# Kernel tuning notes

Hardware: AMD Instinct MI355X
Metric: run time of the kernel (lower is better)

The kernel has to match this reference:

```python
import jax, jax.numpy as jnp
import numpy as np

NC = 80
REG = 16          # DFL bins per coordinate
CONF_THRES = 0.25
IOU_THRES = 0.45
MAX_DET = 300
TOPK = 1000       # fixed-size pre-NMS candidate pool (stand-in for max_nms=30000 with A=8400)
MAX_WH = 7680.0   # class offset for class-aware NMS
LEVELS = [(80, 80, 8.0), (40, 40, 16.0), (20, 20, 32.0)]  # (h, w, stride) for imgsz=640


def _make_anchors():
    """make_anchors: grid-cell centers (+0.5 offset) and per-anchor strides."""
    pts, strs = [], []
    for h, w, s in LEVELS:
        sx = jnp.arange(w, dtype=jnp.float32) + 0.5
        sy = jnp.arange(h, dtype=jnp.float32) + 0.5
        gy, gx = jnp.meshgrid(sy, sx, indexing='ij')
        pts.append(jnp.stack([gx, gy], -1).reshape(-1, 2))
        strs.append(jnp.full((h * w,), s, dtype=jnp.float32))
    return jnp.concatenate(pts).T, jnp.concatenate(strs)  # [2, A], [A]


def _box_iou(b):  # b: [K, 4] xyxy -> [K, K] pairwise IoU
    area = (b[:, 2] - b[:, 0]) * (b[:, 3] - b[:, 1])
    lt = jnp.maximum(b[:, None, :2], b[None, :, :2])
    rb = jnp.minimum(b[:, None, 2:], b[None, :, 2:])
    wh = jnp.clip(rb - lt, 0.0)
    inter = wh[..., 0] * wh[..., 1]
    return inter / (area[:, None] + area[None, :] - inter + 1e-7)


def _nms_keep(iou, valid):
    """Greedy NMS over score-sorted candidates: keep[i] iff valid and no earlier kept box overlaps > thr."""
    K = iou.shape[0]
    idx = jnp.arange(K)
    def body(keep, i):
        sup = jnp.any((iou[i] > IOU_THRES) & keep & (idx < i))
        return keep.at[i].set(valid[i] & jnp.logical_not(sup)), None
    keep, _ = jax.lax.scan(body, jnp.zeros(K, dtype=bool), idx)
    return keep


def _forward(preds, dfl_w):
    B, C, A = preds.shape
    # DFL decode: softmax over 16 bins, expectation with arange(16) weights (the 1x1 conv)
    box_logits = preds[:, :4 * REG].reshape(B, 4, REG, A)
    dist = jnp.einsum('bqra,r->bqa', jax.nn.softmax(box_logits, axis=2), dfl_w)  # [B,4,A] ltrb
    anc, strd = _make_anchors()
    lt, rb = dist[:, :2], dist[:, 2:]
    x1y1 = anc[None] - lt
    x2y2 = anc[None] + rb
    c_xy = (x1y1 + x2y2) / 2
    wh = x2y2 - x1y1
    dbox = jnp.concatenate([c_xy, wh], axis=1) * strd  # dist2bbox(xywh) * stride, [B,4,A]
    cls = jax.nn.sigmoid(preds[:, 4 * REG:])           # [B,NC,A]
    # xywh2xyxy
    cx, cy, w, h = dbox[:, 0], dbox[:, 1], dbox[:, 2], dbox[:, 3]
    boxes = jnp.stack([cx - w / 2, cy - h / 2, cx + w / 2, cy + h / 2], axis=-1)  # [B,A,4]
    conf = jnp.max(cls, axis=1)      # [B,A]
    j = jnp.argmax(cls, axis=1)      # [B,A]
    score = jnp.where(conf > CONF_THRES, conf, -1.0)
    top_s, top_i = jax.lax.top_k(score, TOPK)                               # [B,K]
    tb = jnp.take_along_axis(boxes, top_i[..., None], axis=1)               # [B,K,4]
    tj = jnp.take_along_axis(j, top_i, axis=1)                              # [B,K]
    valid = top_s > CONF_THRES
    ob = tb + (tj.astype(preds.dtype) * MAX_WH)[..., None]                  # class-offset boxes
    iou = jax.vmap(_box_iou)(ob)                                            # [B,K,K]
    keep = jax.vmap(_nms_keep)(iou, valid)                                  # [B,K]
    sel = jnp.where(keep, top_s, -1e9)
    order = jnp.argsort(-sel, axis=1)[:, :MAX_DET]                          # kept, score-sorted
    fb = jnp.take_along_axis(tb, order[..., None], axis=1)
    fs = jnp.take_along_axis(top_s, order, axis=1)
    fj = jnp.take_along_axis(tj, order, axis=1).astype(preds.dtype)
    fv = jnp.take_along_axis(keep, order, axis=1)
    out = jnp.concatenate([fb, fs[..., None], fj[..., None]], axis=-1)
    return out * fv[..., None].astype(preds.dtype)                          # [B,300,6]


def setup_inputs() -> dict:
    key = jax.random.key(0)
    k1, _ = jax.random.split(key)
    preds = jax.random.normal(k1, (32, 4 * REG + NC, 8400), dtype=jnp.float32)
    dfl_w = jnp.arange(REG, dtype=jnp.float32)
    return {"preds": preds, "dfl_w": dfl_w}


def reference(preds, dfl_w):
    return _forward(preds, dfl_w)
```

## Files before the change

### kernel.cpp

```cpp
#include <hip/hip_runtime.h>
#include <cstdint>
#include <cstddef>

typedef unsigned long long u64;
typedef unsigned int u32;

#define A_TOT   8400
#define NCLS    80
#define KSLOT   1024
#define NCHUNK  9
#define TOPK_N  1000
#define MAXDET  300
#define OUT_STRIDE (MAXDET * 6)


__device__ __forceinline__ float sig32(float x) {
#pragma clang fp contract(off)
    float e = (float)exp(-(double)x);
    float t = 1.0f + e;
    return 1.0f / t;
}

__device__ __forceinline__ u32 key_hi_from_score(float s) {
    u32 u = __float_as_uint(s);
    return (u & 0x80000000u) ? ~u : (u | 0x80000000u);
}
__device__ __forceinline__ float score_from_key_hi(u32 t) {
    u32 u = (t & 0x80000000u) ? (t ^ 0x80000000u) : ~t;
    return __uint_as_float(u);
}

__global__ __launch_bounds__(256) void k_decode(const float* __restrict__ preds,
                                                u64* __restrict__ key_raw,
                                                float4* __restrict__ dbox) {
#pragma clang fp contract(off)
    __shared__ float tile[2][16][256];
    int b = blockIdx.y;
    int a0 = blockIdx.x * 256;
    int t = threadIdx.x;
    int a = a0 + t;
    int nA = A_TOT - a0; if (nA > 256) nA = 256;
    int p4max = nA >> 2;
    const float* pb = preds + (size_t)b * 144 * A_TOT;

    int sr[4], sp[4];
#pragma unroll
    for (int k = 0; k < 4; ++k) { int f = t + 256 * k; sr[k] = f >> 6; sp[k] = f & 63; }

    float4 regs[4];
    auto gload = [&](int ch0) {
#pragma unroll
        for (int k = 0; k < 4; ++k) {
            if (sp[k] < p4max)
                regs[k] = *(const float4*)(pb + (size_t)(ch0 + sr[k]) * A_TOT + a0 + 4 * sp[k]);
            else
                regs[k] = make_float4(0.f, 0.f, 0.f, 0.f);
        }
    };
    auto dswrite = [&](int buf) {
#pragma unroll
        for (int k = 0; k < 4; ++k)
            *(float4*)&tile[buf][sr[k]][4 * sp[k]] = regs[k];
    };

    float d[4] = {0.f, 0.f, 0.f, 0.f};
    float m = -3.0e38f, m2 = -3.0e38f;
    int jm = 0;

    gload(0); dswrite(0); __syncthreads();
    gload(16);

    for (int cb = 0; cb < 9; ++cb) {
        int buf = cb & 1;
        if (t < nA) {
            float x[16];
#pragma unroll
            for (int r = 0; r < 16; ++r) x[r] = tile[buf][r][t];
            if (cb < 4) {
                float mx = x[0];
#pragma unroll
                for (int r = 1; r < 16; ++r) mx = fmaxf(mx, x[r]);
                float e[16], s = 0.f;
#pragma unroll
                for (int r = 0; r < 16; ++r) { e[r] = expf(x[r] - mx); s = s + e[r]; }
                float dd = 0.f;
#pragma unroll
                for (int r = 0; r < 16; ++r) { float pr = e[r] / s; dd = dd + pr * (float)r; }
                d[cb] = dd;
            } else {
                int cbase = (cb - 4) * 16;
#pragma unroll
                for (int r = 0; r < 16; ++r) {
                    int c = cbase + r;
                    float v = x[r];
                    if (v > m) { m2 = m; m = v; jm = c; }
                    else if (v > m2) { m2 = v; }
                }
            }
        }
        if (cb + 1 < 9) {
            __syncthreads();
            dswrite((cb + 1) & 1);
            if (cb + 2 < 9) gload((cb + 2) * 16);
            __syncthreads();
        }
    }

    if (t >= nA) return;

    const float* pc = pb + (size_t)64 * A_TOT + a;
    float conf; int cls = jm;
    if ((m - m2) < 1e-4f || m > 7.0f) {
        float sb = -1.0f; int jb = 0;
        for (int c = 0; c < NCLS; ++c) {
            float s = sig32(pc[(size_t)c * A_TOT]);
            if (s > sb) { sb = s; jb = c; }
        }
        conf = sb; cls = jb;
    } else {
        conf = sig32(m);
    }
    float score = (conf > 0.25f) ? conf : -1.0f;
    u32 hi = key_hi_from_score(score);
    u32 lo = ((0x3FFFu - (u32)a) << 7) | (u32)cls;
    key_raw[(size_t)b * A_TOT + a] = ((u64)hi << 32) | lo;

    int row, col; float stride;
    if (a < 6400)      { row = a / 80;          col = a % 80;          stride = 8.0f; }
    else if (a < 8000) { int aa = a - 6400; row = aa / 40; col = aa % 40; stride = 16.0f; }
    else               { int aa = a - 8000; row = aa / 20; col = aa % 20; stride = 32.0f; }
    float ax = (float)col + 0.5f;
    float ay = (float)row + 0.5f;
    float x1 = ax - d[0], y1 = ay - d[1];
    float x2 = ax + d[2], y2 = ay + d[3];
    float cx = (x1 + x2) / 2.0f, cy = (y1 + y2) / 2.0f;
    float w  = x2 - x1,          h  = y2 - y1;
    float4 db;
    db.x = cx * stride; db.y = cy * stride; db.z = w * stride; db.w = h * stride;
    dbox[(size_t)b * A_TOT + a] = db;
}

__global__ __launch_bounds__(1024) void k_chunksort(const u64* __restrict__ key_raw,
                                                    u64* __restrict__ key_sorted) {
    __shared__ u64 s[KSLOT];
    int b = blockIdx.y, ch = blockIdx.x, t = threadIdx.x;
    int a = ch * KSLOT + t;
    s[t] = (a < A_TOT) ? key_raw[(size_t)b * A_TOT + a] : 0ull;
    __syncthreads();
    for (int k = 2; k <= KSLOT; k <<= 1) {
        for (int j = k >> 1; j > 0; j >>= 1) {
            int ixj = t ^ j;
            if (ixj > t) {
                u64 x = s[t], y = s[ixj];
                bool descBlock = ((t & k) == 0);
                bool sw = descBlock ? (x < y) : (x > y);
                if (sw) { s[t] = y; s[ixj] = x; }
            }
            __syncthreads();
        }
    }
    key_sorted[((size_t)b * NCHUNK + ch) * KSLOT + t] = s[t];
}

__global__ __launch_bounds__(1024) void k_merge(const u64* __restrict__ key_sorted,
                                                u64* __restrict__ topk) {
    __shared__ u64 R[KSLOT];
    __shared__ u64 C[KSLOT];
    int b = blockIdx.x, t = threadIdx.x;
    R[t] = key_sorted[((size_t)b * NCHUNK) * KSLOT + t];
    for (int ch = 1; ch < NCHUNK; ++ch) {
        C[t] = key_sorted[((size_t)b * NCHUNK + ch) * KSLOT + t];
        __syncthreads();
        u64 r = R[t];
        u64 c = C[(KSLOT - 1) - t];
        u64 nv = (r > c) ? r : c;
        __syncthreads();
        R[t] = nv;
        __syncthreads();
        for (int j = KSLOT >> 1; j >= 1; j >>= 1) {
            int ixj = t ^ j;
            if (ixj > t) {
                u64 x = R[t], y = R[ixj];
                if (x < y) { R[t] = y; R[ixj] = x; }
            }
            __syncthreads();
        }
    }
    topk[(size_t)b * KSLOT + t] = R[t];
}

__global__ void k_prep(const float4* __restrict__ dbox, const u64* __restrict__ topk,
                       float* __restrict__ tb, float* __restrict__ ob,
                       float* __restrict__ area, u32* __restrict__ validf) {
#pragma clang fp contract(off)
    int slot = blockIdx.x * blockDim.x + threadIdx.x;
    int b = blockIdx.y;
    if (slot >= KSLOT) return;
    size_t si = (size_t)b * KSLOT + slot;
    u64 key = topk[si];
    u32 hi = (u32)(key >> 32);
    u32 lo = (u32)key;
    bool valid = (slot < TOPK_N) && (hi & 0x80000000u);
    if (!valid) {
        tb[si*4+0]=0.f; tb[si*4+1]=0.f; tb[si*4+2]=0.f; tb[si*4+3]=0.f;
        ob[si*4+0]=0.f; ob[si*4+1]=0.f; ob[si*4+2]=0.f; ob[si*4+3]=0.f;
        area[si] = 0.f; validf[si] = 0u;
        return;
    }
    int a   = 0x3FFF - (int)((lo >> 7) & 0x3FFFu);
    int cls = (int)(lo & 0x7Fu);

    float4 db = dbox[(size_t)b * A_TOT + a];
    float bx1 = db.x - db.z / 2.0f, by1 = db.y - db.w / 2.0f;
    float bx2 = db.x + db.z / 2.0f, by2 = db.y + db.w / 2.0f;
    tb[si*4+0] = bx1; tb[si*4+1] = by1; tb[si*4+2] = bx2; tb[si*4+3] = by2;

    float off = (float)cls * 7680.0f;
    float o0 = bx1 + off, o1 = by1 + off, o2 = bx2 + off, o3 = by2 + off;
    ob[si*4+0] = o0; ob[si*4+1] = o1; ob[si*4+2] = o2; ob[si*4+3] = o3;
    area[si] = (o2 - o0) * (o3 - o1);
    validf[si] = 1u;
}

__global__ __launch_bounds__(256) void k_matrix(const float* __restrict__ ob,
                                                const float* __restrict__ area,
                                                u64* __restrict__ masks) {
#pragma clang fp contract(off)
    __shared__ float4 sob[KSLOT];
    __shared__ float  sar[KSLOT];
    int b = blockIdx.y, rblk = blockIdx.x, tid = threadIdx.x;
    const float4* gob = (const float4*)(ob + (size_t)b * KSLOT * 4);
    const float*  gar = area + (size_t)b * KSLOT;
    for (int i = tid; i < KSLOT; i += blockDim.x) { sob[i] = gob[i]; sar[i] = gar[i]; }
    __syncthreads();

    int lane = tid & 63;
    int wave = tid >> 6;
    int i = rblk * 64 + lane;
    float4 bi = sob[i];
    float Ai = sar[i];

#pragma unroll
    for (int wl = 0; wl < 4; ++wl) {
        int w = wave * 4 + wl;
        u64 mword = 0ull;
        if (w >= rblk) {
            for (int bit = 0; bit < 64; ++bit) {
                int j = (w << 6) + bit;
                float4 bj = sob[j];
                float Aj = sar[j];
                float lt0 = fmaxf(bi.x, bj.x);
                float lt1 = fmaxf(bi.y, bj.y);
                float rb0 = fminf(bi.z, bj.z);
                float rb1 = fminf(bi.w, bj.w);
                float ww = fmaxf(rb0 - lt0, 0.0f);
                float hh = fmaxf(rb1 - lt1, 0.0f);
                float inter = ww * hh;
                float den = ((Ai + Aj) - inter) + 1e-7f;
                float iou = inter / den;
                if ((j > i) && (iou > 0.45f)) mword |= (1ull << bit);
            }
        }
        masks[((size_t)b * KSLOT + i) * 16 + w] = mword;
    }
}

__global__ __launch_bounds__(64) void k_scan(const u64* __restrict__ masks,
                                             const u32* __restrict__ validf,
                                             u64* __restrict__ keep) {
    __shared__ u64 rows[KSLOT];
    int b = blockIdx.x, lane = threadIdx.x;
    const char* base = (const char*)(masks + (size_t)b * KSLOT * 16);

    float4 r0, r1, r2, r3, r4, r5, r6, r7;
    {
        const float4* src = (const float4*)base;
        r0 = src[0*64 + lane]; r1 = src[1*64 + lane];
        r2 = src[2*64 + lane]; r3 = src[3*64 + lane];
        r4 = src[4*64 + lane]; r5 = src[5*64 + lane];
        r6 = src[6*64 + lane]; r7 = src[7*64 + lane];
    }

    u64 kw = 0ull;
    u64 rem = 0ull;
    int kept = 0;

    for (int w = 0; w < 16; ++w) {
        {
            float4* dst = (float4*)rows;
            dst[0*64 + lane] = r0; dst[1*64 + lane] = r1;
            dst[2*64 + lane] = r2; dst[3*64 + lane] = r3;
            dst[4*64 + lane] = r4; dst[5*64 + lane] = r5;
            dst[6*64 + lane] = r6; dst[7*64 + lane] = r7;
        }
        u32 vf = validf[(size_t)b * KSLOT + w * 64 + lane];
        u64 valid_w = __ballot(vf != 0u);
        __syncthreads();
        if (w < 15) {
            const float4* src = (const float4*)(base + (size_t)(w + 1) * 8192);
            r0 = src[0*64 + lane]; r1 = src[1*64 + lane];
            r2 = src[2*64 + lane]; r3 = src[3*64 + lane];
            r4 = src[4*64 + lane]; r5 = src[5*64 + lane];
            r6 = src[6*64 + lane]; r7 = src[7*64 + lane];
        }

        u64 live = valid_w & ~__shfl(rem, w);
        while (live) {
            int i = __ffsll(live) - 1;
            if (lane == w) kw |= (1ull << i);
            u64 m = (lane < 16) ? rows[i * 16 + lane] : 0ull;
            rem |= m;
            ++kept;
            if (kept >= MAXDET) break;
            live &= ~(__shfl(m, w) | (1ull << i));
        }
        if (kept >= MAXDET) break;
        __syncthreads();
    }
    if (lane < 16) keep[(size_t)b * 16 + lane] = kw;
}

__global__ __launch_bounds__(1024) void k_final(const u64* __restrict__ keep,
                                                const u64* __restrict__ topk,
                                                const float* __restrict__ tb,
                                                float* __restrict__ out) {
    __shared__ u64 kw[16];
    __shared__ int pref[16];
    int b = blockIdx.x, t = threadIdx.x;
    float* ob_ = out + (size_t)b * OUT_STRIDE;
    for (int i = t; i < OUT_STRIDE; i += blockDim.x) ob_[i] = 0.0f;
    if (t < 16) kw[t] = keep[(size_t)b * 16 + t];
    __syncthreads();
    if (t == 0) {
        int s = 0;
        for (int w = 0; w < 16; ++w) { pref[w] = s; s += __popcll(kw[w]); }
    }
    __syncthreads();
    int w = t >> 6, bit = t & 63;
    bool kp = (kw[w] >> bit) & 1ull;
    if (kp) {
        u64 below = (bit == 0) ? 0ull : (kw[w] & ((1ull << bit) - 1ull));
        int rank = pref[w] + __popcll(below);
        if (rank < MAXDET) {
            size_t si = (size_t)b * KSLOT + t;
            u64 key = topk[si];
            u32 hi = (u32)(key >> 32);
            u32 lo = (u32)key;
            float score = score_from_key_hi(hi);
            float clsf = (float)(lo & 0x7Fu);
            float* o = ob_ + rank * 6;
            o[0] = tb[si*4+0]; o[1] = tb[si*4+1];
            o[2] = tb[si*4+2]; o[3] = tb[si*4+3];
            o[4] = score; o[5] = clsf;
        }
    }
}

extern "C" void kernel_launch(void* const* d_in, const int* in_sizes, int n_in,
                              void* d_out, int out_size, void* d_ws, size_t ws_size,
                              hipStream_t stream) {
    const float* preds = (const float*)d_in[0];
    float* out = (float*)d_out;
    int B = in_sizes[0] / (144 * A_TOT);

    char* ws = (char*)d_ws;
    size_t off = 0;
    u64* key_raw    = (u64*)(ws + off); off += (size_t)B * A_TOT * 8;
    u64* key_sorted = (u64*)(ws + off); off += (size_t)B * NCHUNK * KSLOT * 8;
    u64* topk       = (u64*)(ws + off); off += (size_t)B * KSLOT * 8;
    float4* dbox    = (float4*)(ws + off); off += (size_t)B * A_TOT * 16;
    float* tb       = (float*)(ws + off); off += (size_t)B * KSLOT * 4 * 4;
    float* obuf     = (float*)(ws + off); off += (size_t)B * KSLOT * 4 * 4;
    float* area     = (float*)(ws + off); off += (size_t)B * KSLOT * 4;
    u32* validf     = (u32*)(ws + off); off += (size_t)B * KSLOT * 4;
    u64* masks      = (u64*)(ws + off); off += (size_t)B * KSLOT * 16 * 8;
    u64* keep       = (u64*)(ws + off); off += (size_t)B * 16 * 8;

    k_decode<<<dim3((A_TOT + 255) / 256, B), 256, 0, stream>>>(preds, key_raw, dbox);
    k_chunksort<<<dim3(NCHUNK, B), KSLOT, 0, stream>>>(key_raw, key_sorted);
    k_merge<<<B, KSLOT, 0, stream>>>(key_sorted, topk);
    k_prep<<<dim3(KSLOT / 256, B), 256, 0, stream>>>(dbox, topk, tb, obuf, area, validf);
    k_matrix<<<dim3(16, B), 256, 0, stream>>>(obuf, area, masks);
    k_scan<<<B, 64, 0, stream>>>(masks, validf, keep);
    k_final<<<B, 1024, 0, stream>>>(keep, topk, tb, out);
}
```

Measured before the change: 167.9 us.

## Replace bitonic chunk merge with merge-path tree selection fused with prep

The sequential 8-step bitonic merge of sorted chunks is replaced by a tree of merge-path rank selections. Each thread binary-searches for its output element when merging two sorted lists and keeps the top 1024. The prep kernel is fused into the same kernel, which removes one launch and the topk re-read. The first level reads global memory directly inside the binary search, which adds dependent latency, but far fewer barriers are needed.

```diff
diff --git a/kernel.cpp b/kernel.cpp
--- a/kernel.cpp
+++ b/kernel.cpp
@@ -28,6 +28,18 @@
 __device__ __forceinline__ float score_from_key_hi(u32 t) {
     u32 u = (t & 0x80000000u) ? (t ^ 0x80000000u) : ~t;
     return __uint_as_float(u);
+}
+
+__device__ __forceinline__ u64 mp_rank(const u64* __restrict__ A,
+                                       const u64* __restrict__ B, int t) {
+    int lo = 0, hi = t;
+    while (lo < hi) {
+        int mid = (lo + hi + 1) >> 1;
+        if (A[mid - 1] > B[t - mid]) lo = mid; else hi = mid - 1;
+    }
+    int i = lo, j = t - lo;
+    u64 av = A[i], bv = B[j];
+    return av > bv ? av : bv;
 }
 
 __global__ __launch_bounds__(256) void k_decode(const float* __restrict__ preds,
@@ -162,45 +174,46 @@
     key_sorted[((size_t)b * NCHUNK + ch) * KSLOT + t] = s[t];
 }
 
-__global__ __launch_bounds__(1024) void k_merge(const u64* __restrict__ key_sorted,
-                                                u64* __restrict__ topk) {
-    __shared__ u64 R[KSLOT];
-    __shared__ u64 C[KSLOT];
+__global__ __launch_bounds__(1024) void k_select(const u64* __restrict__ key_sorted,
+                                                 u64* __restrict__ topk,
+                                                 const float4* __restrict__ dbox,
+                                                 float* __restrict__ tb,
+                                                 float* __restrict__ ob,
+                                                 float* __restrict__ area,
+                                                 u32* __restrict__ validf) {
+#pragma clang fp contract(off)
+    __shared__ u64 L[5 * KSLOT];
     int b = blockIdx.x, t = threadIdx.x;
-    R[t] = key_sorted[((size_t)b * NCHUNK) * KSLOT + t];
-    for (int ch = 1; ch < NCHUNK; ++ch) {
-        C[t] = key_sorted[((size_t)b * NCHUNK + ch) * KSLOT + t];
-        __syncthreads();
-        u64 r = R[t];
-        u64 c = C[(KSLOT - 1) - t];
-        u64 nv = (r > c) ? r : c;
-        __syncthreads();
-        R[t] = nv;
-        __syncthreads();
-        for (int j = KSLOT >> 1; j >= 1; j >>= 1) {
-            int ixj = t ^ j;
-            if (ixj > t) {
-                u64 x = R[t], y = R[ixj];
-                if (x < y) { R[t] = y; R[ixj] = x; }
-            }
-            __syncthreads();
-        }
-    }
-    topk[(size_t)b * KSLOT + t] = R[t];
-}
-
-__global__ void k_prep(const float4* __restrict__ dbox, const u64* __restrict__ topk,
-                       float* __restrict__ tb, float* __restrict__ ob,
-                       float* __restrict__ area, u32* __restrict__ validf) {
-#pragma clang fp contract(off)
-    int slot = blockIdx.x * blockDim.x + threadIdx.x;
-    int b = blockIdx.y;
-    if (slot >= KSLOT) return;
-    size_t si = (size_t)b * KSLOT + slot;
-    u64 key = topk[si];
+    const u64* KS = key_sorted + (size_t)b * NCHUNK * KSLOT;
+
+    u64 r0 = mp_rank(KS + 0 * KSLOT, KS + 1 * KSLOT, t);
+    u64 r1 = mp_rank(KS + 2 * KSLOT, KS + 3 * KSLOT, t);
+    u64 r2 = mp_rank(KS + 4 * KSLOT, KS + 5 * KSLOT, t);
+    u64 r3 = mp_rank(KS + 6 * KSLOT, KS + 7 * KSLOT, t);
+    u64 r4 = KS[8 * KSLOT + t];
+    L[0 * KSLOT + t] = r0; L[1 * KSLOT + t] = r1;
+    L[2 * KSLOT + t] = r2; L[3 * KSLOT + t] = r3;
+    L[4 * KSLOT + t] = r4;
+    __syncthreads();
+
+    u64 m0 = mp_rank(L + 0 * KSLOT, L + 1 * KSLOT, t);
+    u64 m1 = mp_rank(L + 2 * KSLOT, L + 3 * KSLOT, t);
+    __syncthreads();
+    L[0 * KSLOT + t] = m0; L[1 * KSLOT + t] = m1;
+    __syncthreads();
+
+    u64 s0 = mp_rank(L + 0 * KSLOT, L + 1 * KSLOT, t);
+    __syncthreads();
+    L[0 * KSLOT + t] = s0;
+    __syncthreads();
+
+    u64 key = mp_rank(L + 0 * KSLOT, L + 4 * KSLOT, t);
+    size_t si = (size_t)b * KSLOT + t;
+    topk[si] = key;
+
     u32 hi = (u32)(key >> 32);
     u32 lo = (u32)key;
-    bool valid = (slot < TOPK_N) && (hi & 0x80000000u);
+    bool valid = (t < TOPK_N) && (hi & 0x80000000u);
     if (!valid) {
         tb[si*4+0]=0.f; tb[si*4+1]=0.f; tb[si*4+2]=0.f; tb[si*4+3]=0.f;
         ob[si*4+0]=0.f; ob[si*4+1]=0.f; ob[si*4+2]=0.f; ob[si*4+3]=0.f;
@@ -378,8 +391,7 @@
 
     k_decode<<<dim3((A_TOT + 255) / 256, B), 256, 0, stream>>>(preds, key_raw, dbox);
     k_chunksort<<<dim3(NCHUNK, B), KSLOT, 0, stream>>>(key_raw, key_sorted);
-    k_merge<<<B, KSLOT, 0, stream>>>(key_sorted, topk);
-    k_prep<<<dim3(KSLOT / 256, B), 256, 0, stream>>>(dbox, topk, tb, obuf, area, validf);
+    k_select<<<B, KSLOT, 0, stream>>>(key_sorted, topk, dbox, tb, obuf, area, validf);
     k_matrix<<<dim3(16, B), 256, 0, stream>>>(obuf, area, masks);
     k_scan<<<B, 64, 0, stream>>>(masks, validf, keep);
     k_final<<<B, 1024, 0, stream>>>(keep, topk, tb, out);
```

Result: no change. 167.4 us (-0.3%).
